# Performance work log

Hardware: AMD Instinct MI355X
Metric: run time of the kernel (lower is better)

The kernel has to match this reference:

```python
import jax, jax.numpy as jnp
import numpy as np

GAMMA = 0.999   # from TDLoss.__init__ default
LAMBDA = 0.95   # from compute_gae default lambda_
B, S = 8192, 2048


def setup_inputs() -> dict:
    key = jax.random.key(0)
    k1, k2, k3, k4 = jax.random.split(key, 4)
    rewards = jax.random.normal(k1, (B, S), dtype=jnp.float32)
    values = jax.random.normal(k2, (B, S), dtype=jnp.float32)
    dones = jax.random.randint(k3, (B, S), 0, 2).astype(jnp.int32)
    # prefix validity mask: valid_len[b] = mask[b].sum(), as assumed by compute_gae
    lengths = jax.random.randint(k4, (B,), S // 2, S + 1)
    mask = (jnp.arange(S)[None, :] < lengths[:, None]).astype(jnp.int32)
    return {"rewards": rewards, "values": values, "dones": dones, "mask": mask}


def _gae(rewards, values, dones_f, mask, gamma, lam):
    # rewards/values/dones_f: [B,S] float; mask: [B,S] int prefix mask
    b, s = rewards.shape
    valid_len = mask.sum(axis=1)                      # [B]
    t_idx = jnp.arange(s)
    valid = t_idx[None, :] < valid_len[:, None]       # [B,S] bool
    is_last = t_idx[None, :] == (valid_len[:, None] - 1)
    # next_value = values[:, t+1], except 0 at the last valid step (and at t=S-1)
    next_vals = jnp.concatenate([values[:, 1:], jnp.zeros((b, 1), values.dtype)], axis=1)
    next_vals = jnp.where(is_last, jnp.zeros((), values.dtype), next_vals)
    nd = 1.0 - dones_f                                # (1 - done)
    delta = rewards + gamma * next_vals * nd - values

    def step(gae, xs):
        d_t, nd_t, valid_t = xs                        # each [B]
        g = d_t + gamma * lam * nd_t * gae
        g = jnp.where(valid_t, g, jnp.zeros((), d_t.dtype))  # zero outside valid prefix; resets carry
        return g, g

    xs = (delta.T, nd.T, valid.T)                     # time-major [S,B]
    _, adv_t = jax.lax.scan(step, jnp.zeros(b, rewards.dtype), xs, reverse=True)
    advantages = adv_t.T                              # [B,S]
    returns = jnp.where(valid, advantages + values, jnp.zeros((), values.dtype))
    return advantages, returns


def reference(rewards, values, dones, mask):
    return _gae(rewards, values, dones.astype(jnp.float32), mask, GAMMA, LAMBDA)
```

## Files before the change

kernel.cpp:

```cpp
#include <hip/hip_runtime.h>


static constexpr int BATCH = 8192;
static constexpr int SEQ   = 2048;
static constexpr int CHUNK = SEQ / 64;
static constexpr float GAMMA  = 0.999f;
static constexpr float LAMBDA = 0.95f;
static constexpr float GL     = GAMMA * LAMBDA;

__global__ __launch_bounds__(256, 2) void gae_kernel(
    const float* __restrict__ rewards,
    const float* __restrict__ values,
    const int*   __restrict__ dones,
    const int*   __restrict__ mask,
    float*       __restrict__ out)
{
    const int lane = threadIdx.x & 63;
    const int row  = blockIdx.x * (blockDim.x >> 6) + (threadIdx.x >> 6);
    if (row >= BATCH) return;

    const size_t base = (size_t)row * SEQ + (size_t)lane * CHUNK;

    float a[CHUNK], b[CHUNK], vmm[CHUNK];

    const float4* rp = reinterpret_cast<const float4*>(rewards + base);
    const float4* vp = reinterpret_cast<const float4*>(values  + base);
    const int4*   dp = reinterpret_cast<const int4*>(dones + base);
    const int4*   mp = reinterpret_cast<const int4*>(mask  + base);

    float pend_mr = 0.f, pend_mnd = 0.f, pend_vmm = 0.f;

    #pragma unroll
    for (int q = 0; q < CHUNK / 4; ++q) {
        float4 r4 = rp[q];
        float4 v4 = vp[q];
        int4   d4 = dp[q];
        int4   m4 = mp[q];
        float rr[4]  = {r4.x, r4.y, r4.z, r4.w};
        float vv[4]  = {v4.x, v4.y, v4.z, v4.w};
        float dd[4]  = {(float)d4.x, (float)d4.y, (float)d4.z, (float)d4.w};
        float mm[4]  = {(float)m4.x, (float)m4.y, (float)m4.z, (float)m4.w};
        #pragma unroll
        for (int j = 0; j < 4; ++j) {
            const int k = 4 * q + j;
            const float m   = mm[j];
            const float nd  = 1.0f - dd[j];
            const float mnd = m * nd;
            vmm[k] = m * vv[j];
            a[k]   = GL * mnd;
            if (k > 0) {
                b[k - 1] = pend_mr + GAMMA * vmm[k] * pend_mnd - pend_vmm;
            }
            pend_mr  = m * rr[j];
            pend_mnd = mnd;
            pend_vmm = vmm[k];
        }
    }
    float nv_edge = __shfl_down(vmm[0], 1, 64);
    if (lane == 63) nv_edge = 0.0f;
    b[CHUNK - 1] = pend_mr + GAMMA * nv_edge * pend_mnd - pend_vmm;

    float A = 1.0f, Bc = 0.0f;
    #pragma unroll
    for (int k = CHUNK - 1; k >= 0; --k) {
        Bc = fmaf(a[k], Bc, b[k]);
        A  = a[k] * A;
    }

    #pragma unroll
    for (int d = 1; d < 64; d <<= 1) {
        float Ao = __shfl_down(A,  d, 64);
        float Bo = __shfl_down(Bc, d, 64);
        if (lane + d < 64) {
            Bc = fmaf(A, Bo, Bc);
            A  = A * Ao;
        }
    }
    float carry = __shfl_down(Bc, 1, 64);
    if (lane == 63) carry = 0.0f;

    float g = carry;
    #pragma unroll
    for (int k = CHUNK - 1; k >= 0; --k) {
        g = fmaf(a[k], g, b[k]);
        b[k]   = g;
        vmm[k] = vmm[k] + g;
    }

    float4* ap = reinterpret_cast<float4*>(out + base);
    float4* tp = reinterpret_cast<float4*>(out + (size_t)BATCH * SEQ + base);
    #pragma unroll
    for (int q = 0; q < CHUNK / 4; ++q) {
        ap[q] = make_float4(b[4*q+0],   b[4*q+1],   b[4*q+2],   b[4*q+3]);
        tp[q] = make_float4(vmm[4*q+0], vmm[4*q+1], vmm[4*q+2], vmm[4*q+3]);
    }
}

extern "C" void kernel_launch(void* const* d_in, const int* in_sizes, int n_in,
                              void* d_out, int out_size, void* d_ws, size_t ws_size,
                              hipStream_t stream) {
    const float* rewards = (const float*)d_in[0];
    const float* values  = (const float*)d_in[1];
    const int*   dones   = (const int*)d_in[2];
    const int*   mask    = (const int*)d_in[3];
    float* out = (float*)d_out;

    const int rows_per_block = 256 / 64;
    dim3 grid(BATCH / rows_per_block), block(256);
    gae_kernel<<<grid, block, 0, stream>>>(rewards, values, dones, mask, out);
}
```

Before: 332.4 us.

## Process each row in coalesced 256-element tiles with carried affine scan

```diff
diff --git a/kernel.cpp b/kernel.cpp
--- a/kernel.cpp
+++ b/kernel.cpp
@@ -3,12 +3,13 @@
 
 static constexpr int BATCH = 8192;
 static constexpr int SEQ   = 2048;
-static constexpr int CHUNK = SEQ / 64;
+static constexpr int TBLK  = 256;
+static constexpr int NBLK  = SEQ / TBLK;
 static constexpr float GAMMA  = 0.999f;
 static constexpr float LAMBDA = 0.95f;
 static constexpr float GL     = GAMMA * LAMBDA;
 
-__global__ __launch_bounds__(256, 2) void gae_kernel(
+__global__ __launch_bounds__(256, 4) void gae_kernel(
     const float* __restrict__ rewards,
     const float* __restrict__ values,
     const int*   __restrict__ dones,
@@ -16,83 +17,82 @@
     float*       __restrict__ out)
 {
     const int lane = threadIdx.x & 63;
-    const int row  = blockIdx.x * (blockDim.x >> 6) + (threadIdx.x >> 6);
-    if (row >= BATCH) return;
+    const int row  = blockIdx.x * 4 + (threadIdx.x >> 6);
+    const size_t rowbase = (size_t)row * SEQ;
 
-    const size_t base = (size_t)row * SEQ + (size_t)lane * CHUNK;
+    float C    = 0.0f;
+    float edge = 0.0f;
 
-    float a[CHUNK], b[CHUNK], vmm[CHUNK];
+    for (int j = NBLK - 1; j >= 0; --j) {
+        const size_t off = rowbase + (size_t)j * TBLK + (size_t)lane * 4;
 
-    const float4* rp = reinterpret_cast<const float4*>(rewards + base);
-    const float4* vp = reinterpret_cast<const float4*>(values  + base);
-    const int4*   dp = reinterpret_cast<const int4*>(dones + base);
-    const int4*   mp = reinterpret_cast<const int4*>(mask  + base);
+        const float4 r4 = *reinterpret_cast<const float4*>(rewards + off);
+        const float4 v4 = *reinterpret_cast<const float4*>(values  + off);
+        const int4   d4 = *reinterpret_cast<const int4*>(dones + off);
+        const int4   m4 = *reinterpret_cast<const int4*>(mask  + off);
 
-    float pend_mr = 0.f, pend_mnd = 0.f, pend_vmm = 0.f;
+        const float rr[4] = {r4.x, r4.y, r4.z, r4.w};
+        const float vv[4] = {v4.x, v4.y, v4.z, v4.w};
+        const int   dd[4] = {d4.x, d4.y, d4.z, d4.w};
+        const int   mm[4] = {m4.x, m4.y, m4.z, m4.w};
 
-    #pragma unroll
-    for (int q = 0; q < CHUNK / 4; ++q) {
-        float4 r4 = rp[q];
-        float4 v4 = vp[q];
-        int4   d4 = dp[q];
-        int4   m4 = mp[q];
-        float rr[4]  = {r4.x, r4.y, r4.z, r4.w};
-        float vv[4]  = {v4.x, v4.y, v4.z, v4.w};
-        float dd[4]  = {(float)d4.x, (float)d4.y, (float)d4.z, (float)d4.w};
-        float mm[4]  = {(float)m4.x, (float)m4.y, (float)m4.z, (float)m4.w};
+        float a[4], b[4], vm[4];
+        float mr[4], mnd[4];
         #pragma unroll
-        for (int j = 0; j < 4; ++j) {
-            const int k = 4 * q + j;
-            const float m   = mm[j];
-            const float nd  = 1.0f - dd[j];
-            const float mnd = m * nd;
-            vmm[k] = m * vv[j];
-            a[k]   = GL * mnd;
-            if (k > 0) {
-                b[k - 1] = pend_mr + GAMMA * vmm[k] * pend_mnd - pend_vmm;
+        for (int e = 0; e < 4; ++e) {
+            const bool m  = (mm[e] != 0);
+            const bool mn = m && (dd[e] == 0);
+            vm[e]  = m ? vv[e] : 0.0f;
+            mr[e]  = m ? rr[e] : 0.0f;
+            mnd[e] = mn ? 1.0f : 0.0f;
+            a[e]   = mn ? GL : 0.0f;
+        }
+        float nv3 = __shfl_down(vm[0], 1, 64);
+        if (lane == 63) nv3 = edge;
+        const float nv[4] = {vm[1], vm[2], vm[3], nv3};
+        #pragma unroll
+        for (int e = 0; e < 4; ++e)
+            b[e] = mr[e] + GAMMA * nv[e] * mnd[e] - vm[e];
+
+        float A = a[3], B = b[3];
+        #pragma unroll
+        for (int e = 2; e >= 0; --e) {
+            B = fmaf(a[e], B, b[e]);
+            A = a[e] * A;
+        }
+
+        float As = A, Bs = B;
+        #pragma unroll
+        for (int d = 1; d < 64; d <<= 1) {
+            const float Ao = __shfl_down(As, d, 64);
+            const float Bo = __shfl_down(Bs, d, 64);
+            if (lane + d < 64) {
+                Bs = fmaf(As, Bo, Bs);
+                As = As * Ao;
             }
-            pend_mr  = m * rr[j];
-            pend_mnd = mnd;
-            pend_vmm = vmm[k];
         }
-    }
-    float nv_edge = __shfl_down(vmm[0], 1, 64);
-    if (lane == 63) nv_edge = 0.0f;
-    b[CHUNK - 1] = pend_mr + GAMMA * nv_edge * pend_mnd - pend_vmm;
+        const float A0 = __shfl(As, 0, 64);
+        const float B0 = __shfl(Bs, 0, 64);
+        float cA = __shfl_down(As, 1, 64);
+        float cB = __shfl_down(Bs, 1, 64);
+        if (lane == 63) { cA = 1.0f; cB = 0.0f; }
+        float g = fmaf(cA, C, cB);
 
-    float A = 1.0f, Bc = 0.0f;
-    #pragma unroll
-    for (int k = CHUNK - 1; k >= 0; --k) {
-        Bc = fmaf(a[k], Bc, b[k]);
-        A  = a[k] * A;
-    }
+        float adv[4], ret[4];
+        #pragma unroll
+        for (int e = 3; e >= 0; --e) {
+            g = fmaf(a[e], g, b[e]);
+            adv[e] = g;
+            ret[e] = g + vm[e];
+        }
 
-    #pragma unroll
-    for (int d = 1; d < 64; d <<= 1) {
-        float Ao = __shfl_down(A,  d, 64);
-        float Bo = __shfl_down(Bc, d, 64);
-        if (lane + d < 64) {
-            Bc = fmaf(A, Bo, Bc);
-            A  = A * Ao;
-        }
-    }
-    float carry = __shfl_down(Bc, 1, 64);
-    if (lane == 63) carry = 0.0f;
+        C    = fmaf(A0, C, B0);
+        edge = __shfl(vm[0], 0, 64);
 
-    float g = carry;
-    #pragma unroll
-    for (int k = CHUNK - 1; k >= 0; --k) {
-        g = fmaf(a[k], g, b[k]);
-        b[k]   = g;
-        vmm[k] = vmm[k] + g;
-    }
-
-    float4* ap = reinterpret_cast<float4*>(out + base);
-    float4* tp = reinterpret_cast<float4*>(out + (size_t)BATCH * SEQ + base);
-    #pragma unroll
-    for (int q = 0; q < CHUNK / 4; ++q) {
-        ap[q] = make_float4(b[4*q+0],   b[4*q+1],   b[4*q+2],   b[4*q+3]);
-        tp[q] = make_float4(vmm[4*q+0], vmm[4*q+1], vmm[4*q+2], vmm[4*q+3]);
+        *reinterpret_cast<float4*>(out + off) =
+            make_float4(adv[0], adv[1], adv[2], adv[3]);
+        *reinterpret_cast<float4*>(out + (size_t)BATCH * SEQ + off) =
+            make_float4(ret[0], ret[1], ret[2], ret[3]);
     }
 }
 
@@ -105,7 +105,6 @@
     const int*   mask    = (const int*)d_in[3];
     float* out = (float*)d_out;
 
-    const int rows_per_block = 256 / 64;
-    dim3 grid(BATCH / rows_per_block), block(256);
+    dim3 grid(BATCH / 4), block(256);
     gae_kernel<<<grid, block, 0, stream>>>(rewards, values, dones, mask, out);
 }
```

Result: faster. 320.3 us (-3.6%).
